# Kernel optimization log

Hardware: AMD Instinct MI355X
Metric: run time of the kernel (lower is better)

## Reference

```python
import jax, jax.numpy as jnp
import numpy as np

N_NODES = 100000
N_EDGES = 20000
N_INC = 800000


def hconv(node_idx, edge_idx, X, w, W, b):
    # node -> hyperedge: weighted mean of member node features
    msg = X[node_idx] * w[node_idx, None]                      # [I, d]
    e_sum = jax.ops.segment_sum(msg, edge_idx, num_segments=N_EDGES)
    e_den = jax.ops.segment_sum(w[node_idx], edge_idx, num_segments=N_EDGES)
    e_feat = e_sum / jnp.maximum(e_den, 1e-6)[:, None]         # [E, d]
    # hyperedge -> node: mean over incident hyperedges
    v_sum = jax.ops.segment_sum(e_feat[edge_idx], node_idx, num_segments=N_NODES)
    v_deg = jax.ops.segment_sum(jnp.ones((edge_idx.shape[0],), X.dtype),
                                node_idx, num_segments=N_NODES)
    v_feat = v_sum / jnp.maximum(v_deg, 1.0)[:, None]          # [N, d]
    return v_feat @ W + b


def setup_inputs() -> dict:
    key = jax.random.key(0)
    k1, k2, k3, k4, k5, k6 = jax.random.split(key, 6)
    d, h, c = 256, 16, 40
    H = jax.random.normal(k1, (N_NODES, d), dtype=jnp.float32)
    input_weight = jax.random.uniform(k2, (N_NODES,), dtype=jnp.float32)
    node_idx = jax.random.randint(k3, (N_INC,), 0, N_NODES, dtype=jnp.int32)
    edge_idx = jax.random.randint(k4, (N_INC,), 0, N_EDGES, dtype=jnp.int32)
    W1 = jax.random.normal(k5, (d, h), dtype=jnp.float32) / np.sqrt(d)
    b1 = jnp.zeros((h,), jnp.float32)
    W2 = jax.random.normal(k6, (h, c), dtype=jnp.float32) / np.sqrt(h)
    b2 = jnp.zeros((c,), jnp.float32)
    return {"H": H, "input_weight": input_weight, "node_idx": node_idx,
            "edge_idx": edge_idx, "W1": W1, "b1": b1, "W2": W2, "b2": b2}


def reference(H, input_weight, node_idx, edge_idx, W1, b1, W2, b2):
    x = jax.nn.relu(hconv(node_idx, edge_idx, H, input_weight, W1, b1))
    # dropout is identity at inference (training=False)
    x = hconv(node_idx, edge_idx, x, input_weight, W2, b2)
    return jax.nn.log_softmax(x, axis=1)
```

## Files before the change

### kernel.cpp

```cpp
#include <hip/hip_runtime.h>

#define N_NODES 100000
#define N_EDGES 20000
#define N_INC   800000
#define D_IN    256
#define D_H     16
#define D_OUT   40

#define EBS    32
#define NBE    625
#define ECAP   1600
#define VBS    256
#define NBV    392
#define VCAP   2400
#define TE     4096
#define EPART  196
#define TV     6144
#define NPART  131
#define GEMM_BLOCKS 782

typedef short bf16x8 __attribute__((ext_vector_type(8)));
typedef float f32x4  __attribute__((ext_vector_type(4)));

__device__ __forceinline__ unsigned short f2bf(float f) {
    unsigned u = __float_as_uint(f);
    unsigned r = u + 0x7FFF + ((u >> 16) & 1);
    return (unsigned short)(r >> 16);
}

__global__ __launch_bounds__(512) void init_kernel(
    const float* __restrict__ W1, unsigned short* __restrict__ bfrag,
    int* __restrict__ cnts ) {
    int t = threadIdx.x;
    for (int i = t; i < 1032; i += 512) cnts[i] = 0;
    int c = t >> 6, l = t & 63;
    int n = l & 15, q = l >> 4;
    unsigned short v[8];
#pragma unroll
    for (int j = 0; j < 8; ++j)
        v[j] = f2bf(W1[(c * 32 + q * 8 + j) * D_H + n]);
    *(int4*)(bfrag + (size_t)(c * 64 + l) * 8) = *(int4*)v;
}

union SMemP {
    struct { int lrec[TE]; int lhist[NBE]; int lbase[NBE];
             int gbase[NBE]; int lcur[NBE]; int sc[512]; } pe;
    struct { int lrec[TV]; int lhist[NBV]; int lbase[NBV];
             int gbase[NBV]; int lcur[NBV]; int sc[512]; } pn;
};

__global__ __launch_bounds__(512) void part_gemm_kernel(
    const int* __restrict__ ni, const int* __restrict__ ei,
    const float* __restrict__ w,
    int* __restrict__ cnt_be, int* __restrict__ cnt_bv,
    int* __restrict__ staged_e, int* __restrict__ staged_v,
    const float* __restrict__ H, const unsigned short* __restrict__ bfrag,
    float* __restrict__ T) {
    __shared__ SMemP sm;
    int t = threadIdx.x;
    if (blockIdx.x < EPART) {
        int base = blockIdx.x * TE;
        for (int i = t; i < NBE; i += 512) sm.pe.lhist[i] = 0;
        __syncthreads();
#pragma unroll
        for (int r = 0; r < TE / 512; ++r) {
            int idx = base + r * 512 + t;
            if (idx < N_INC) atomicAdd(&sm.pe.lhist[ei[idx] >> 5], 1);
        }
        __syncthreads();
        int b0 = 2 * t, b1 = 2 * t + 1;
        int h0 = (b0 < NBE) ? sm.pe.lhist[b0] : 0;
        int h1 = (b1 < NBE) ? sm.pe.lhist[b1] : 0;
        int local = h0 + h1;
        sm.pe.sc[t] = local; __syncthreads();
        for (int o = 1; o < 512; o <<= 1) {
            int x = (t >= o) ? sm.pe.sc[t - o] : 0; __syncthreads();
            sm.pe.sc[t] += x; __syncthreads();
        }
        int ex = sm.pe.sc[t] - local;
        if (b0 < NBE) {
            sm.pe.lbase[b0] = ex; sm.pe.lcur[b0] = ex;
            sm.pe.gbase[b0] = h0 ? (b0 * ECAP + atomicAdd(&cnt_be[b0], h0)) : 0;
        }
        if (b1 < NBE) {
            int ex1 = ex + h0;
            sm.pe.lbase[b1] = ex1; sm.pe.lcur[b1] = ex1;
            sm.pe.gbase[b1] = h1 ? (b1 * ECAP + atomicAdd(&cnt_be[b1], h1)) : 0;
        }
        __syncthreads();
#pragma unroll
        for (int r = 0; r < TE / 512; ++r) {
            int idx = base + r * 512 + t;
            if (idx < N_INC) {
                int e = ei[idx], v = ni[idx];
                int key = e >> 5;
                int rec = v | ((e & 31) << 17) | (key << 22);
                int p = atomicAdd(&sm.pe.lcur[key], 1);
                sm.pe.lrec[p] = rec;
            }
        }
        __syncthreads();
        int total = min(TE, N_INC - base);
        for (int i = t; i < total; i += 512) {
            int rec = sm.pe.lrec[i];
            int bk = ((unsigned)rec) >> 22;
            int dst = sm.pe.gbase[bk] + (i - sm.pe.lbase[bk]);
            if (dst < (bk + 1) * ECAP) staged_e[dst] = rec;
        }
    } else if (blockIdx.x < EPART + NPART) {
        int base = (blockIdx.x - EPART) * TV;
        for (int i = t; i < NBV; i += 512) sm.pn.lhist[i] = 0;
        __syncthreads();
#pragma unroll
        for (int r = 0; r < TV / 512; ++r) {
            int idx = base + r * 512 + t;
            if (idx < N_INC) atomicAdd(&sm.pn.lhist[ni[idx] >> 8], 1);
        }
        __syncthreads();
        int h = (t < NBV) ? sm.pn.lhist[t] : 0;
        sm.pn.sc[t] = h; __syncthreads();
        for (int o = 1; o < 512; o <<= 1) {
            int x = (t >= o) ? sm.pn.sc[t - o] : 0; __syncthreads();
            sm.pn.sc[t] += x; __syncthreads();
        }
        if (t < NBV) {
            int ex = sm.pn.sc[t] - h;
            sm.pn.lbase[t] = ex; sm.pn.lcur[t] = ex;
            sm.pn.gbase[t] = h ? (t * VCAP + atomicAdd(&cnt_bv[t], h)) : 0;
        }
        __syncthreads();
#pragma unroll
        for (int r = 0; r < TV / 512; ++r) {
            int idx = base + r * 512 + t;
            if (idx < N_INC) {
                int e = ei[idx], v = ni[idx];
                int key = v >> 8;
                int rec = e | ((v & 255) << 15) | (key << 23);
                int p = atomicAdd(&sm.pn.lcur[key], 1);
                sm.pn.lrec[p] = rec;
            }
        }
        __syncthreads();
        int total = min(TV, N_INC - base);
        for (int i = t; i < total; i += 512) {
            int rec = sm.pn.lrec[i];
            int bk = ((unsigned)rec) >> 23;
            int dst = sm.pn.gbase[bk] + (i - sm.pn.lbase[bk]);
            if (dst < (bk + 1) * VCAP) staged_v[dst] = rec;
        }
    } else {
        int wave = ((blockIdx.x - EPART - NPART) * 512 + t) >> 6;
        if (wave >= N_NODES / 16) return;
        int lane = t & 63;
        int m = lane & 15, q = lane >> 4;
        int row0 = wave * 16;
        const float* hp = H + (size_t)(row0 + m) * D_IN + q * 8;
        bf16x8 bf[8];
        const int4* bp = (const int4*)bfrag;
#pragma unroll
        for (int c = 0; c < 8; ++c) {
            int4 raw = bp[c * 64 + lane];
            bf[c] = *(bf16x8*)&raw;
        }
        f32x4 acc = {0.f, 0.f, 0.f, 0.f};
#pragma unroll
        for (int c = 0; c < 8; ++c) {
            float4 lo = *(const float4*)(hp + c * 32);
            float4 hi = *(const float4*)(hp + c * 32 + 4);
            bf16x8 af;
            af[0] = f2bf(lo.x); af[1] = f2bf(lo.y); af[2] = f2bf(lo.z); af[3] = f2bf(lo.w);
            af[4] = f2bf(hi.x); af[5] = f2bf(hi.y); af[6] = f2bf(hi.z); af[7] = f2bf(hi.w);
            acc = __builtin_amdgcn_mfma_f32_16x16x32_bf16(af, bf[c], acc, 0, 0, 0);
        }
#pragma unroll
        for (int r = 0; r < 4; ++r) {
            int row = row0 + q * 4 + r;
            T[(size_t)row * D_H + m] = acc[r] * w[row];
        }
    }
}

__global__ __launch_bounds__(512) void mega2e_kernel(
    const int* __restrict__ cnt_be, int* __restrict__ staged_e,
    int2* __restrict__ off_e2) {
    __shared__ int lsort[ECAP];
    __shared__ int hist[EBS], cursor[EBS];
    int b = blockIdx.x, t = threadIdx.x;
    int beg = b * ECAP, cnt = min(cnt_be[b], ECAP);
    if (t < EBS) hist[t] = 0;
    __syncthreads();
    int rec[4], key[4], nr = 0;
#pragma unroll
    for (int r = 0; r < 4; ++r) {
        int k = r * 512 + t;
        if (k < cnt) {
            rec[nr] = staged_e[beg + k];
            key[nr] = (rec[nr] >> 17) & 31;
            atomicAdd(&hist[key[nr]], 1);
            ++nr;
        }
    }
    __syncthreads();
    if (t < EBS) {
        int hh = hist[t], s = hh;
#pragma unroll
        for (int o = 1; o < EBS; o <<= 1) {
            int x = __shfl_up(s, o, 64);
            if (t >= o) s += x;
        }
        int ex = s - hh;
        cursor[t] = ex;
        off_e2[b * EBS + t] = make_int2(beg + ex, beg + ex + hh);
    }
    __syncthreads();
    for (int r = 0; r < nr; ++r) {
        int p = atomicAdd(&cursor[key[r]], 1);
        lsort[p] = rec[r];
    }
    __syncthreads();
    for (int i = t; i < cnt; i += 512) staged_e[beg + i] = lsort[i];
}

__global__ __launch_bounds__(512) void m2n_gA1_kernel(
    const int* __restrict__ cnt_bv, int* __restrict__ staged_v,
    int2* __restrict__ off_v2,
    const int2* __restrict__ off_e2, const int* __restrict__ staged_e,
    const float* __restrict__ T, const float* __restrict__ w,
    float* __restrict__ e_den, float* __restrict__ e_feat) {
    __shared__ int lsort[VCAP];
    __shared__ int hist[VBS], cursor[VBS], sc[512];
    int t = threadIdx.x;
    if (blockIdx.x < NBV) {
        int b = blockIdx.x;
        int beg = b * VCAP, cnt = min(cnt_bv[b], VCAP);
        for (int i = t; i < VBS; i += 512) hist[i] = 0;
        __syncthreads();
        int rec[5], key[5], nr = 0;
#pragma unroll
        for (int r = 0; r < 5; ++r) {
            int k = r * 512 + t;
            if (k < cnt) {
                rec[nr] = staged_v[beg + k];
                key[nr] = (rec[nr] >> 15) & 255;
                atomicAdd(&hist[key[nr]], 1);
                ++nr;
            }
        }
        __syncthreads();
        int hh = (t < VBS) ? hist[t] : 0;
        sc[t] = hh; __syncthreads();
        for (int o = 1; o < 512; o <<= 1) {
            int x = (t >= o) ? sc[t - o] : 0; __syncthreads();
            sc[t] += x; __syncthreads();
        }
        if (t < VBS) {
            int ex = sc[t] - hh;
            cursor[t] = ex;
            int n = b * VBS + t;
            if (n < N_NODES) off_v2[n] = make_int2(beg + ex, beg + ex + hh);
        }
        __syncthreads();
        for (int r = 0; r < nr; ++r) {
            int p = atomicAdd(&cursor[key[r]], 1);
            lsort[p] = rec[r];
        }
        __syncthreads();
        for (int i = t; i < cnt; i += 512) staged_v[beg + i] = lsort[i];
    } else {
        int e = ((blockIdx.x - NBV) * 512 + t) >> 6;
        if (e >= N_EDGES) return;
        int lane = t & 63;
        int g = lane >> 2, c = (lane & 3) << 2;
        int2 be = off_e2[e];
        f32x4 acc = {0.f, 0.f, 0.f, 0.f};
        float den = 0.f;
        for (int k = be.x + g; k < be.y; k += 16) {
            int rec = staged_e[k];
            int v = rec & 0x1FFFF;
            acc += *(const f32x4*)(T + (size_t)v * D_H + c);
            if ((lane & 3) == 0) den += w[v];
        }
#pragma unroll
        for (int s = 4; s <= 32; s <<= 1) {
            acc[0] += __shfl_xor(acc[0], s, 64);
            acc[1] += __shfl_xor(acc[1], s, 64);
            acc[2] += __shfl_xor(acc[2], s, 64);
            acc[3] += __shfl_xor(acc[3], s, 64);
            den    += __shfl_xor(den,    s, 64);
        }
        den = __shfl(den, 0, 64);
        if (lane == 0) e_den[e] = den;
        float inv = 1.f / fmaxf(den, 1e-6f);
        if (lane < 4) {
            f32x4 r = acc * inv;
            *(f32x4*)(e_feat + (size_t)e * D_H + c) = r;
        }
    }
}

__global__ __launch_bounds__(512) void gatherA2_kernel(
    const int2* __restrict__ off_e2, const int* __restrict__ staged_e,
    const float* __restrict__ X, const float* __restrict__ e_den,
    float* __restrict__ e_feat) {
    int e = (blockIdx.x * 512 + threadIdx.x) >> 6;
    if (e >= N_EDGES) return;
    int lane = threadIdx.x & 63;
    int g = lane >> 2, c = (lane & 3) << 2;
    int2 be = off_e2[e];
    f32x4 acc = {0.f, 0.f, 0.f, 0.f};
    for (int k = be.x + g; k < be.y; k += 16) {
        int rec = staged_e[k];
        int v = rec & 0x1FFFF;
        acc += *(const f32x4*)(X + (size_t)v * D_H + c);
    }
#pragma unroll
    for (int s = 4; s <= 32; s <<= 1) {
        acc[0] += __shfl_xor(acc[0], s, 64);
        acc[1] += __shfl_xor(acc[1], s, 64);
        acc[2] += __shfl_xor(acc[2], s, 64);
        acc[3] += __shfl_xor(acc[3], s, 64);
    }
    if (lane < 4) {
        float inv = 1.f / fmaxf(e_den[e], 1e-6f);
        f32x4 r = acc * inv;
        *(f32x4*)(e_feat + (size_t)e * D_H + c) = r;
    }
}

__global__ __launch_bounds__(512) void gatherB1_kernel(
    const int2* __restrict__ off_v2, const int* __restrict__ staged_v,
    const float* __restrict__ e_feat, const float* __restrict__ w,
    const float* __restrict__ b1, float* __restrict__ out) {
    int t = blockIdx.x * 512 + threadIdx.x;
    int n = t >> 2;
    if (n >= N_NODES) return;
    int c = (t & 3) << 2;
    int2 be = off_v2[n];
    f32x4 acc = {0.f, 0.f, 0.f, 0.f};
    for (int k = be.x; k < be.y; ++k) {
        int e = staged_v[k] & 0x7FFF;
        acc += *(const f32x4*)(e_feat + (size_t)e * D_H + c);
    }
    float inv = 1.f / fmaxf((float)(be.y - be.x), 1.f);
    f32x4 bb = *(const f32x4*)(b1 + c);
    float wn = w[n];
    f32x4 r;
#pragma unroll
    for (int i = 0; i < 4; ++i) r[i] = fmaxf(acc[i] * inv + bb[i], 0.f) * wn;
    *(f32x4*)(out + (size_t)n * D_H + c) = r;
}

__global__ __launch_bounds__(512) void gatherB2_final_kernel(
    const int2* __restrict__ off_v2, const int* __restrict__ staged_v,
    const float* __restrict__ e_feat,
    const float* __restrict__ W2, const float* __restrict__ b2,
    float* __restrict__ out) {
    __shared__ float sy[128 * 20];
    __shared__ float sW2[D_H * D_OUT];
    __shared__ float sb2[D_OUT];
    int t = threadIdx.x;
    for (int i = t; i < D_H * D_OUT; i += 512) sW2[i] = W2[i];
    if (t < D_OUT) sb2[t] = b2[t];
    int nl = t >> 2, c = (t & 3) << 2;
    int n = blockIdx.x * 128 + nl;
    f32x4 y = {0.f, 0.f, 0.f, 0.f};
    if (n < N_NODES) {
        int2 be = off_v2[n];
        f32x4 acc = {0.f, 0.f, 0.f, 0.f};
        for (int k = be.x; k < be.y; ++k) {
            int e = staged_v[k] & 0x7FFF;
            acc += *(const f32x4*)(e_feat + (size_t)e * D_H + c);
        }
        float inv = 1.f / fmaxf((float)(be.y - be.x), 1.f);
        y = acc * inv;
    }
    *(f32x4*)(sy + nl * 20 + c) = y;
    __syncthreads();
    if (n >= N_NODES) return;
    int c0 = (t & 3) * 10;
    float z[10];
#pragma unroll
    for (int i = 0; i < 10; ++i) z[i] = sb2[c0 + i];
#pragma unroll
    for (int jj = 0; jj < D_H; ++jj) {
        float yy = sy[nl * 20 + jj];
#pragma unroll
        for (int i = 0; i < 10; ++i) z[i] += yy * sW2[jj * D_OUT + c0 + i];
    }
    float m = z[0];
#pragma unroll
    for (int i = 1; i < 10; ++i) m = fmaxf(m, z[i]);
    m = fmaxf(m, __shfl_xor(m, 1, 64));
    m = fmaxf(m, __shfl_xor(m, 2, 64));
    float se = 0.f;
#pragma unroll
    for (int i = 0; i < 10; ++i) se += __expf(z[i] - m);
    se += __shfl_xor(se, 1, 64);
    se += __shfl_xor(se, 2, 64);
    float lse = m + __logf(se);
    float* op = out + (size_t)n * D_OUT + c0;
#pragma unroll
    for (int i = 0; i < 10; ++i) op[i] = z[i] - lse;
}

extern "C" void kernel_launch(void* const* d_in, const int* in_sizes, int n_in,
                              void* d_out, int out_size, void* d_ws, size_t ws_size,
                              hipStream_t stream) {
    const float* H  = (const float*)d_in[0];
    const float* w  = (const float*)d_in[1];
    const int*   ni = (const int*)d_in[2];
    const int*   ei = (const int*)d_in[3];
    const float* W1 = (const float*)d_in[4];
    const float* b1 = (const float*)d_in[5];
    const float* W2 = (const float*)d_in[6];
    const float* b2 = (const float*)d_in[7];
    float* out = (float*)d_out;

    int*            ws_i     = (int*)d_ws;
    int*            cnt_be   = ws_i + 0;
    int*            cnt_bv   = ws_i + 640;
    unsigned short* bfrag    = (unsigned short*)(ws_i + 1040);
    int2*           off_e2   = (int2*)(ws_i + 3088);
    int2*           off_v2   = (int2*)(ws_i + 43088);
    int*            staged_e = ws_i + 243088;
    int*            staged_v = ws_i + 1243088;
    float*          e_den    = (float*)(ws_i + 2183888);
    float*          T        = (float*)(ws_i + 2203888);
    float*          e_feat   = (float*)(ws_i + 3803888);
    float*          x1       = (float*)(ws_i + 4123888);

    init_kernel<<<1, 512, 0, stream>>>(W1, bfrag, cnt_be);

    part_gemm_kernel<<<EPART + NPART + GEMM_BLOCKS, 512, 0, stream>>>(
        ni, ei, w, cnt_be, cnt_bv, staged_e, staged_v, H, bfrag, T);

    mega2e_kernel<<<NBE, 512, 0, stream>>>(cnt_be, staged_e, off_e2);

    m2n_gA1_kernel<<<NBV + 2500, 512, 0, stream>>>(
        cnt_bv, staged_v, off_v2, off_e2, staged_e, T, w, e_den, e_feat);

    gatherB1_kernel<<<782, 512, 0, stream>>>(off_v2, staged_v, e_feat, w, b1, x1);

    gatherA2_kernel<<<2500, 512, 0, stream>>>(off_e2, staged_e, x1, e_den, e_feat);

    gatherB2_final_kernel<<<782, 512, 0, stream>>>(
        off_v2, staged_v, e_feat, W2, b2, out);
}
```

Before: 249.6 us.

## Fuse edge-bucket sort with first edge gather and replace barrier scans with wave scans

Merges the edge-bucket sort kernel and the first node-to-hyperedge gather into one kernel. Each block sorts its 32 edges in shared memory and immediately gathers the T rows for those edges, with 16 threads per edge. The node-bucket sort runs in the same launch, which removes one kernel launch and a global re-read of the staged edge records. The 512-step shared-memory Hillis-Steele scans with many barriers are replaced by a wave-shuffle scan plus per-wave totals. GEMM blocks are moved to the front of the partition launch so they get scheduled first. The fused gather uses a scalar 16-lane layout with 4-way unrolling, which may give different load efficiency than the previous vectorized per-wave gather.

```diff
diff --git a/kernel.cpp b/kernel.cpp
--- a/kernel.cpp
+++ b/kernel.cpp
@@ -28,11 +28,27 @@
     return (unsigned short)(r >> 16);
 }
 
+__device__ __forceinline__ int block_exscan512(int local, int* sc8) {
+    int t = threadIdx.x, lane = t & 63, wid = t >> 6;
+    int s = local;
+#pragma unroll
+    for (int o = 1; o < 64; o <<= 1) {
+        int x = __shfl_up(s, o, 64);
+        if (lane >= o) s += x;
+    }
+    if (lane == 63) sc8[wid] = s;
+    __syncthreads();
+    int wbase = 0;
+#pragma unroll
+    for (int i = 0; i < 8; ++i) if (i < wid) wbase += sc8[i];
+    return wbase + s - local;
+}
+
 __global__ __launch_bounds__(512) void init_kernel(
     const float* __restrict__ W1, unsigned short* __restrict__ bfrag,
     int* __restrict__ cnts ) {
     int t = threadIdx.x;
-    for (int i = t; i < 1032; i += 512) cnts[i] = 0;
+    for (int i = t; i < 1040; i += 512) cnts[i] = 0;
     int c = t >> 6, l = t & 63;
     int n = l & 15, q = l >> 4;
     unsigned short v[8];
@@ -44,9 +60,9 @@
 
 union SMemP {
     struct { int lrec[TE]; int lhist[NBE]; int lbase[NBE];
-             int gbase[NBE]; int lcur[NBE]; int sc[512]; } pe;
+             int gbase[NBE]; int lcur[NBE]; int sc[8]; } pe;
     struct { int lrec[TV]; int lhist[NBV]; int lbase[NBV];
-             int gbase[NBV]; int lcur[NBV]; int sc[512]; } pn;
+             int gbase[NBV]; int lcur[NBV]; int sc[8]; } pn;
 };
 
 __global__ __launch_bounds__(512) void part_gemm_kernel(
@@ -58,8 +74,37 @@
     float* __restrict__ T) {
     __shared__ SMemP sm;
     int t = threadIdx.x;
-    if (blockIdx.x < EPART) {
-        int base = blockIdx.x * TE;
+    if (blockIdx.x < GEMM_BLOCKS) {
+        int wave = (blockIdx.x * 512 + t) >> 6;
+        if (wave >= N_NODES / 16) return;
+        int lane = t & 63;
+        int m = lane & 15, q = lane >> 4;
+        int row0 = wave * 16;
+        const float* hp = H + (size_t)(row0 + m) * D_IN + q * 8;
+        bf16x8 bf[8];
+        const int4* bp = (const int4*)bfrag;
+#pragma unroll
+        for (int c = 0; c < 8; ++c) {
+            int4 raw = bp[c * 64 + lane];
+            bf[c] = *(bf16x8*)&raw;
+        }
+        f32x4 acc = {0.f, 0.f, 0.f, 0.f};
+#pragma unroll
+        for (int c = 0; c < 8; ++c) {
+            float4 lo = *(const float4*)(hp + c * 32);
+            float4 hi = *(const float4*)(hp + c * 32 + 4);
+            bf16x8 af;
+            af[0] = f2bf(lo.x); af[1] = f2bf(lo.y); af[2] = f2bf(lo.z); af[3] = f2bf(lo.w);
+            af[4] = f2bf(hi.x); af[5] = f2bf(hi.y); af[6] = f2bf(hi.z); af[7] = f2bf(hi.w);
+            acc = __builtin_amdgcn_mfma_f32_16x16x32_bf16(af, bf[c], acc, 0, 0, 0);
+        }
+#pragma unroll
+        for (int r = 0; r < 4; ++r) {
+            int row = row0 + q * 4 + r;
+            T[(size_t)row * D_H + m] = acc[r] * w[row];
+        }
+    } else if (blockIdx.x < GEMM_BLOCKS + EPART) {
+        int base = (blockIdx.x - GEMM_BLOCKS) * TE;
         for (int i = t; i < NBE; i += 512) sm.pe.lhist[i] = 0;
         __syncthreads();
 #pragma unroll
@@ -71,13 +116,7 @@
         int b0 = 2 * t, b1 = 2 * t + 1;
         int h0 = (b0 < NBE) ? sm.pe.lhist[b0] : 0;
         int h1 = (b1 < NBE) ? sm.pe.lhist[b1] : 0;
-        int local = h0 + h1;
-        sm.pe.sc[t] = local; __syncthreads();
-        for (int o = 1; o < 512; o <<= 1) {
-            int x = (t >= o) ? sm.pe.sc[t - o] : 0; __syncthreads();
-            sm.pe.sc[t] += x; __syncthreads();
-        }
-        int ex = sm.pe.sc[t] - local;
+        int ex = block_exscan512(h0 + h1, sm.pe.sc);
         if (b0 < NBE) {
             sm.pe.lbase[b0] = ex; sm.pe.lcur[b0] = ex;
             sm.pe.gbase[b0] = h0 ? (b0 * ECAP + atomicAdd(&cnt_be[b0], h0)) : 0;
@@ -107,8 +146,8 @@
             int dst = sm.pe.gbase[bk] + (i - sm.pe.lbase[bk]);
             if (dst < (bk + 1) * ECAP) staged_e[dst] = rec;
         }
-    } else if (blockIdx.x < EPART + NPART) {
-        int base = (blockIdx.x - EPART) * TV;
+    } else {
+        int base = (blockIdx.x - GEMM_BLOCKS - EPART) * TV;
         for (int i = t; i < NBV; i += 512) sm.pn.lhist[i] = 0;
         __syncthreads();
 #pragma unroll
@@ -118,13 +157,8 @@
         }
         __syncthreads();
         int h = (t < NBV) ? sm.pn.lhist[t] : 0;
-        sm.pn.sc[t] = h; __syncthreads();
-        for (int o = 1; o < 512; o <<= 1) {
-            int x = (t >= o) ? sm.pn.sc[t - o] : 0; __syncthreads();
-            sm.pn.sc[t] += x; __syncthreads();
-        }
+        int ex = block_exscan512(h, sm.pn.sc);
         if (t < NBV) {
-            int ex = sm.pn.sc[t] - h;
             sm.pn.lbase[t] = ex; sm.pn.lcur[t] = ex;
             sm.pn.gbase[t] = h ? (t * VCAP + atomicAdd(&cnt_bv[t], h)) : 0;
         }
@@ -148,92 +182,85 @@
             int dst = sm.pn.gbase[bk] + (i - sm.pn.lbase[bk]);
             if (dst < (bk + 1) * VCAP) staged_v[dst] = rec;
         }
-    } else {
-        int wave = ((blockIdx.x - EPART - NPART) * 512 + t) >> 6;
-        if (wave >= N_NODES / 16) return;
-        int lane = t & 63;
-        int m = lane & 15, q = lane >> 4;
-        int row0 = wave * 16;
-        const float* hp = H + (size_t)(row0 + m) * D_IN + q * 8;
-        bf16x8 bf[8];
-        const int4* bp = (const int4*)bfrag;
-#pragma unroll
-        for (int c = 0; c < 8; ++c) {
-            int4 raw = bp[c * 64 + lane];
-            bf[c] = *(bf16x8*)&raw;
-        }
-        f32x4 acc = {0.f, 0.f, 0.f, 0.f};
-#pragma unroll
-        for (int c = 0; c < 8; ++c) {
-            float4 lo = *(const float4*)(hp + c * 32);
-            float4 hi = *(const float4*)(hp + c * 32 + 4);
-            bf16x8 af;
-            af[0] = f2bf(lo.x); af[1] = f2bf(lo.y); af[2] = f2bf(lo.z); af[3] = f2bf(lo.w);
-            af[4] = f2bf(hi.x); af[5] = f2bf(hi.y); af[6] = f2bf(hi.z); af[7] = f2bf(hi.w);
-            acc = __builtin_amdgcn_mfma_f32_16x16x32_bf16(af, bf[c], acc, 0, 0, 0);
-        }
-#pragma unroll
-        for (int r = 0; r < 4; ++r) {
-            int row = row0 + q * 4 + r;
-            T[(size_t)row * D_H + m] = acc[r] * w[row];
-        }
-    }
-}
-
-__global__ __launch_bounds__(512) void mega2e_kernel(
+    }
+}
+
+union SMemS {
+    struct { int lsort[ECAP]; int hist[EBS]; int cursor[EBS]; int lbeg[EBS]; } e;
+    struct { int lsort[VCAP]; int hist[VBS]; int cursor[VBS]; int sc[8]; } v;
+};
+
+__global__ __launch_bounds__(512) void sortE_gA1_sortN_kernel(
     const int* __restrict__ cnt_be, int* __restrict__ staged_e,
-    int2* __restrict__ off_e2) {
-    __shared__ int lsort[ECAP];
-    __shared__ int hist[EBS], cursor[EBS];
-    int b = blockIdx.x, t = threadIdx.x;
-    int beg = b * ECAP, cnt = min(cnt_be[b], ECAP);
-    if (t < EBS) hist[t] = 0;
-    __syncthreads();
-    int rec[4], key[4], nr = 0;
-#pragma unroll
-    for (int r = 0; r < 4; ++r) {
-        int k = r * 512 + t;
-        if (k < cnt) {
-            rec[nr] = staged_e[beg + k];
-            key[nr] = (rec[nr] >> 17) & 31;
-            atomicAdd(&hist[key[nr]], 1);
-            ++nr;
-        }
-    }
-    __syncthreads();
-    if (t < EBS) {
-        int hh = hist[t], s = hh;
-#pragma unroll
-        for (int o = 1; o < EBS; o <<= 1) {
-            int x = __shfl_up(s, o, 64);
-            if (t >= o) s += x;
-        }
-        int ex = s - hh;
-        cursor[t] = ex;
-        off_e2[b * EBS + t] = make_int2(beg + ex, beg + ex + hh);
-    }
-    __syncthreads();
-    for (int r = 0; r < nr; ++r) {
-        int p = atomicAdd(&cursor[key[r]], 1);
-        lsort[p] = rec[r];
-    }
-    __syncthreads();
-    for (int i = t; i < cnt; i += 512) staged_e[beg + i] = lsort[i];
-}
-
-__global__ __launch_bounds__(512) void m2n_gA1_kernel(
+    int2* __restrict__ off_e2,
     const int* __restrict__ cnt_bv, int* __restrict__ staged_v,
     int2* __restrict__ off_v2,
-    const int2* __restrict__ off_e2, const int* __restrict__ staged_e,
     const float* __restrict__ T, const float* __restrict__ w,
     float* __restrict__ e_den, float* __restrict__ e_feat) {
-    __shared__ int lsort[VCAP];
-    __shared__ int hist[VBS], cursor[VBS], sc[512];
+    __shared__ SMemS sm;
     int t = threadIdx.x;
-    if (blockIdx.x < NBV) {
+    if (blockIdx.x < NBE) {
         int b = blockIdx.x;
+        int beg = b * ECAP, cnt = min(cnt_be[b], ECAP);
+        if (t < EBS) sm.e.hist[t] = 0;
+        __syncthreads();
+        int rec[4], key[4], nr = 0;
+#pragma unroll
+        for (int r = 0; r < 4; ++r) {
+            int k = r * 512 + t;
+            if (k < cnt) {
+                rec[nr] = staged_e[beg + k];
+                key[nr] = (rec[nr] >> 17) & 31;
+                atomicAdd(&sm.e.hist[key[nr]], 1);
+                ++nr;
+            }
+        }
+        __syncthreads();
+        if (t < EBS) {
+            int hh = sm.e.hist[t], s = hh;
+#pragma unroll
+            for (int o = 1; o < EBS; o <<= 1) {
+                int x = __shfl_up(s, o, 64);
+                if (t >= o) s += x;
+            }
+            int ex = s - hh;
+            sm.e.cursor[t] = ex; sm.e.lbeg[t] = ex;
+            off_e2[b * EBS + t] = make_int2(beg + ex, beg + ex + hh);
+        }
+        __syncthreads();
+        for (int r = 0; r < nr; ++r) {
+            int p = atomicAdd(&sm.e.cursor[key[r]], 1);
+            sm.e.lsort[p] = rec[r];
+        }
+        __syncthreads();
+        for (int i = t; i < cnt; i += 512) staged_e[beg + i] = sm.e.lsort[i];
+        int el = t >> 4, j = t & 15;
+        int lo = sm.e.lbeg[el], hi = lo + sm.e.hist[el];
+        float acc = 0.f;
+        int k = lo;
+        for (; k + 4 <= hi; k += 4) {
+            int r0 = sm.e.lsort[k]     & 0x1FFFF;
+            int r1 = sm.e.lsort[k + 1] & 0x1FFFF;
+            int r2 = sm.e.lsort[k + 2] & 0x1FFFF;
+            int r3 = sm.e.lsort[k + 3] & 0x1FFFF;
+            float t0 = T[(size_t)r0 * D_H + j];
+            float t1 = T[(size_t)r1 * D_H + j];
+            float t2 = T[(size_t)r2 * D_H + j];
+            float t3 = T[(size_t)r3 * D_H + j];
+            acc += t0; acc += t1; acc += t2; acc += t3;
+        }
+        for (; k < hi; ++k) acc += T[(size_t)(sm.e.lsort[k] & 0x1FFFF) * D_H + j];
+        float den = 0.f;
+        for (int k2 = lo + j; k2 < hi; k2 += 16) den += w[sm.e.lsort[k2] & 0x1FFFF];
+#pragma unroll
+        for (int o = 1; o < 16; o <<= 1) den += __shfl_xor(den, o, 64);
+        int e = b * EBS + el;
+        e_feat[(size_t)e * D_H + j] = acc / fmaxf(den, 1e-6f);
+        if (j == 0) e_den[e] = den;
+    } else {
+        int b = blockIdx.x - NBE;
         int beg = b * VCAP, cnt = min(cnt_bv[b], VCAP);
-        for (int i = t; i < VBS; i += 512) hist[i] = 0;
+        for (int i = t; i < VBS; i += 512) sm.v.hist[i] = 0;
         __syncthreads();
         int rec[5], key[5], nr = 0;
 #pragma unroll
@@ -242,60 +269,49 @@
             if (k < cnt) {
                 rec[nr] = staged_v[beg + k];
                 key[nr] = (rec[nr] >> 15) & 255;
-                atomicAdd(&hist[key[nr]], 1);
+                atomicAdd(&sm.v.hist[key[nr]], 1);
                 ++nr;
             }
         }
         __syncthreads();
-        int hh = (t < VBS) ? hist[t] : 0;
-        sc[t] = hh; __syncthreads();
-        for (int o = 1; o < 512; o <<= 1) {
-            int x = (t >= o) ? sc[t - o] : 0; __syncthreads();
-            sc[t] += x; __syncthreads();
-        }
+        int hh = (t < VBS) ? sm.v.hist[t] : 0;
+        int ex = block_exscan512(hh, sm.v.sc);
         if (t < VBS) {
-            int ex = sc[t] - hh;
-            cursor[t] = ex;
+            sm.v.cursor[t] = ex;
             int n = b * VBS + t;
             if (n < N_NODES) off_v2[n] = make_int2(beg + ex, beg + ex + hh);
         }
         __syncthreads();
         for (int r = 0; r < nr; ++r) {
-            int p = atomicAdd(&cursor[key[r]], 1);
-            lsort[p] = rec[r];
-        }
-        __syncthreads();
-        for (int i = t; i < cnt; i += 512) staged_v[beg + i] = lsort[i];
-    } else {
-        int e = ((blockIdx.x - NBV) * 512 + t) >> 6;
-        if (e >= N_EDGES) return;
-        int lane = t & 63;
-        int g = lane >> 2, c = (lane & 3) << 2;
-        int2 be = off_e2[e];
-        f32x4 acc = {0.f, 0.f, 0.f, 0.f};
-        float den = 0.f;
-        for (int k = be.x + g; k < be.y; k += 16) {
-            int rec = staged_e[k];
-            int v = rec & 0x1FFFF;
-            acc += *(const f32x4*)(T + (size_t)v * D_H + c);
-            if ((lane & 3) == 0) den += w[v];
-        }
-#pragma unroll
-        for (int s = 4; s <= 32; s <<= 1) {
-            acc[0] += __shfl_xor(acc[0], s, 64);
-            acc[1] += __shfl_xor(acc[1], s, 64);
-            acc[2] += __shfl_xor(acc[2], s, 64);
-            acc[3] += __shfl_xor(acc[3], s, 64);
-            den    += __shfl_xor(den,    s, 64);
-        }
-        den = __shfl(den, 0, 64);
-        if (lane == 0) e_den[e] = den;
-        float inv = 1.f / fmaxf(den, 1e-6f);
-        if (lane < 4) {
-            f32x4 r = acc * inv;
-            *(f32x4*)(e_feat + (size_t)e * D_H + c) = r;
-        }
-    }
+            int p = atomicAdd(&sm.v.cursor[key[r]], 1);
+            sm.v.lsort[p] = rec[r];
+        }
+        __syncthreads();
+        for (int i = t; i < cnt; i += 512) staged_v[beg + i] = sm.v.lsort[i];
+    }
+}
+
+__global__ __launch_bounds__(512) void gatherB1_kernel(
+    const int2* __restrict__ off_v2, const int* __restrict__ staged_v,
+    const float* __restrict__ e_feat, const float* __restrict__ w,
+    const float* __restrict__ b1, float* __restrict__ out) {
+    int t = blockIdx.x * 512 + threadIdx.x;
+    int n = t >> 2;
+    if (n >= N_NODES) return;
+    int c = (t & 3) << 2;
+    int2 be = off_v2[n];
+    f32x4 acc = {0.f, 0.f, 0.f, 0.f};
+    for (int k = be.x; k < be.y; ++k) {
+        int e = staged_v[k] & 0x7FFF;
+        acc += *(const f32x4*)(e_feat + (size_t)e * D_H + c);
+    }
+    float inv = 1.f / fmaxf((float)(be.y - be.x), 1.f);
+    f32x4 bb = *(const f32x4*)(b1 + c);
+    float wn = w[n];
+    f32x4 r;
+#pragma unroll
+    for (int i = 0; i < 4; ++i) r[i] = fmaxf(acc[i] * inv + bb[i], 0.f) * wn;
+    *(f32x4*)(out + (size_t)n * D_H + c) = r;
 }
 
 __global__ __launch_bounds__(512) void gatherA2_kernel(
@@ -325,29 +341,6 @@
         f32x4 r = acc * inv;
         *(f32x4*)(e_feat + (size_t)e * D_H + c) = r;
     }
-}
-
-__global__ __launch_bounds__(512) void gatherB1_kernel(
-    const int2* __restrict__ off_v2, const int* __restrict__ staged_v,
-    const float* __restrict__ e_feat, const float* __restrict__ w,
-    const float* __restrict__ b1, float* __restrict__ out) {
-    int t = blockIdx.x * 512 + threadIdx.x;
-    int n = t >> 2;
-    if (n >= N_NODES) return;
-    int c = (t & 3) << 2;
-    int2 be = off_v2[n];
-    f32x4 acc = {0.f, 0.f, 0.f, 0.f};
-    for (int k = be.x; k < be.y; ++k) {
-        int e = staged_v[k] & 0x7FFF;
-        acc += *(const f32x4*)(e_feat + (size_t)e * D_H + c);
-    }
-    float inv = 1.f / fmaxf((float)(be.y - be.x), 1.f);
-    f32x4 bb = *(const f32x4*)(b1 + c);
-    float wn = w[n];
-    f32x4 r;
-#pragma unroll
-    for (int i = 0; i < 4; ++i) r[i] = fmaxf(acc[i] * inv + bb[i], 0.f) * wn;
-    *(f32x4*)(out + (size_t)n * D_H + c) = r;
 }
 
 __global__ __launch_bounds__(512) void gatherB2_final_kernel(
@@ -431,13 +424,11 @@
 
     init_kernel<<<1, 512, 0, stream>>>(W1, bfrag, cnt_be);
 
-    part_gemm_kernel<<<EPART + NPART + GEMM_BLOCKS, 512, 0, stream>>>(
+    part_gemm_kernel<<<GEMM_BLOCKS + EPART + NPART, 512, 0, stream>>>(
         ni, ei, w, cnt_be, cnt_bv, staged_e, staged_v, H, bfrag, T);
 
-    mega2e_kernel<<<NBE, 512, 0, stream>>>(cnt_be, staged_e, off_e2);
-
-    m2n_gA1_kernel<<<NBV + 2500, 512, 0, stream>>>(
-        cnt_bv, staged_v, off_v2, off_e2, staged_e, T, w, e_den, e_feat);
+    sortE_gA1_sortN_kernel<<<NBE + NBV, 512, 0, stream>>>(
+        cnt_be, staged_e, off_e2, cnt_bv, staged_v, off_v2, T, w, e_den, e_feat);
 
     gatherB1_kernel<<<782, 512, 0, stream>>>(off_v2, staged_v, e_feat, w, b1, x1);
 
```

Measured after the change: 247.2 us. Within noise of the previous version (-0.9%).
